# Kernel optimization log

Hardware: AMD Instinct MI355X
Metric: run time of the kernel (lower is better)

Reference implementation:

```python
import jax, jax.numpy as jnp
import numpy as np

B, T, H, V, ADIM, AMAX = 16, 1024, 512, 32000, 512, 10


def setup_inputs() -> dict:
    key = jax.random.key(0)
    ks = jax.random.split(key, 24)
    def n(k, shape, s=0.05):
        return jax.random.normal(k, shape, jnp.float32) * s
    return {
        "instruction": jax.random.randint(ks[0], (B, T), 0, V, dtype=jnp.int32),
        "emb": n(ks[1], (V, H)),
        "wih_f": n(ks[2], (4 * H, H)), "whh_f": n(ks[3], (4 * H, H)),
        "bih_f": n(ks[4], (4 * H,)), "bhh_f": n(ks[5], (4 * H,)),
        "wih_b": n(ks[6], (4 * H, H)), "whh_b": n(ks[7], (4 * H, H)),
        "bih_b": n(ks[8], (4 * H,)), "bhh_b": n(ks[9], (4 * H,)),
        "wg": n(ks[10], (2 * H, 2 * H)), "bg": n(ks[11], (2 * H,)),
        "ws1": n(ks[12], (H, 2 * H)), "bs1": n(ks[13], (H,)),
        "ws2": n(ks[14], (1, H)), "bs2": n(ks[15], (1,)),
        "wd1": n(ks[16], (H, 2 * H)), "bd1": n(ks[17], (H,)),
        "wd2": n(ks[18], (ADIM, H)), "bd2": n(ks[19], (ADIM,)),
        "max_actions": AMAX,
    }


def _lstm(x, wih, whh, bias):
    # x: [B, T, H] -> outputs [B, T, H]; PyTorch gate order i, f, g, o
    h0 = jnp.zeros((x.shape[0], whh.shape[1]), x.dtype)
    def step(carry, xt):
        h, c = carry
        g = xt @ wih.T + h @ whh.T + bias
        i, f, gg, o = jnp.split(g, 4, axis=-1)
        c = jax.nn.sigmoid(f) * c + jax.nn.sigmoid(i) * jnp.tanh(gg)
        h = jax.nn.sigmoid(o) * jnp.tanh(c)
        return (h, c), h
    _, hs = jax.lax.scan(step, (h0, h0), jnp.swapaxes(x, 0, 1))
    return jnp.swapaxes(hs, 0, 1)


def reference(instruction, emb, wih_f, whh_f, bih_f, bhh_f, wih_b, whh_b, bih_b, bhh_b,
              wg, bg, ws1, bs1, ws2, bs2, wd1, bd1, wd2, bd2, max_actions):
    x = emb[instruction]                                   # [B, T, H]
    fwd = _lstm(x, wih_f, whh_f, bih_f + bhh_f)            # [B, T, H]
    bwd = _lstm(x[:, ::-1], wih_b, whh_b, bih_b + bhh_b)[:, ::-1]
    enc = jnp.concatenate([fwd, bwd], axis=-1)             # [B, T, 2H]
    # sequence_lengths=None: h_n[0]=fwd last step, h_n[1]=bwd at t=0
    pooled = jnp.concatenate([fwd[:, -1], bwd[:, 0]], axis=-1)
    gctx = pooled @ wg.T + bg                               # [B, 2H]
    sh = jax.nn.relu(enc @ ws1.T + bs1)
    seg_probs = jax.nn.sigmoid((sh @ ws2.T + bs2)[..., 0])  # [B, T]
    mask = seg_probs > 0.5
    count = mask.sum(axis=-1)
    # first max_actions True positions per row (stable sort keeps time order)
    order = jnp.argsort(jnp.logical_not(mask), axis=1, stable=True)[:, :max_actions]
    gathered = jnp.take_along_axis(enc, order[..., None], axis=1)  # [B, A, 2H]
    slots = jnp.arange(max_actions)
    valid = slots[None, :] < jnp.minimum(count, max_actions)[:, None]
    empty = ((count == 0)[:, None]) & (slots[None, :] == 0)  # fallback: decode global ctx
    dec_in = jnp.where(valid[..., None], gathered, 0.0)
    dec_in = jnp.where(empty[..., None], gctx[:, None, :], dec_in)
    dh = jax.nn.relu(dec_in @ wd1.T + bd1)
    actions = (dh @ wd2.T + bd2) * (valid | empty)[..., None].astype(dec_in.dtype)
    return actions, seg_probs
```

## Files before the change

kernel.cpp:

```cpp
#include <hip/hip_runtime.h>
#include <math.h>

#define T   1024
#define NB  16
#define HD  512

#define OFF_BAR  0
#define OFF_HH   256
#define OFF_SH   (OFF_HH + 16777216)
#define OFF_SEGP (OFF_SH + 8388608)
#define OFF_GCTX (OFF_SEGP + 16384)
#define OFF_SEL  (OFF_GCTX + 16384)

typedef unsigned long long u64;

__device__ __forceinline__ float sigmoidf_(float x){ return 1.0f/(1.0f + __expf(-x)); }
__device__ __forceinline__ float tanhf_(float x){ return 1.0f - 2.0f/(1.0f + __expf(2.0f*x)); }

__global__ __launch_bounds__(512, 1)
void lstm_kernel(const int* __restrict__ instr, const float* __restrict__ emb,
                 const float* __restrict__ wih_f, const float* __restrict__ whh_f,
                 const float* __restrict__ bih_f, const float* __restrict__ bhh_f,
                 const float* __restrict__ wih_b, const float* __restrict__ whh_b,
                 const float* __restrict__ bih_b, const float* __restrict__ bhh_b,
                 float* __restrict__ ws)
{
    float* h_hist = ws + OFF_HH;
    int* flags = (int*)ws;

    const int wg     = blockIdx.x;
    const int dir    = wg & 1;
    const int bgrp   = (wg >> 1) & 3;
    const int uslice = wg >> 3;
    const int U      = uslice * 16;
    const int b0     = bgrp * 4;

    int* barf = flags + (dir*4 + bgrp)*32;

    const float* wih = dir ? wih_b : wih_f;
    const float* whh = dir ? whh_b : whh_f;
    const float* bih = dir ? bih_b : bih_f;
    const float* bhh = dir ? bhh_b : bhh_f;

    const int tid  = threadIdx.x;
    const int wid  = tid >> 6;
    const int lane = tid & 63;
    const int rg   = wid;

    float wi[64], wh[64];
#pragma unroll
    for (int ri = 0; ri < 8; ++ri){
        int rgl = rg*8 + ri;
        int gate = rgl >> 4, ul = rgl & 15;
        size_t row = (size_t)(gate*HD + U + ul) * HD + lane*8;
        float4 a0 = *(const float4*)(wih + row);
        float4 a1 = *(const float4*)(wih + row + 4);
        float4 b0v = *(const float4*)(whh + row);
        float4 b1v = *(const float4*)(whh + row + 4);
        wi[ri*8+0]=a0.x; wi[ri*8+1]=a0.y; wi[ri*8+2]=a0.z; wi[ri*8+3]=a0.w;
        wi[ri*8+4]=a1.x; wi[ri*8+5]=a1.y; wi[ri*8+6]=a1.z; wi[ri*8+7]=a1.w;
        wh[ri*8+0]=b0v.x; wh[ri*8+1]=b0v.y; wh[ri*8+2]=b0v.z; wh[ri*8+3]=b0v.w;
        wh[ri*8+4]=b1v.x; wh[ri*8+5]=b1v.y; wh[ri*8+6]=b1v.z; wh[ri*8+7]=b1v.w;
    }

    float bI, bF, bG, bO, cst = 0.0f;
    {
        int u = tid & 15;
        bI = bih[0*HD + U + u] + bhh[0*HD + U + u];
        bF = bih[1*HD + U + u] + bhh[1*HD + U + u];
        bG = bih[2*HD + U + u] + bhh[2*HD + U + u];
        bO = bih[3*HD + U + u] + bhh[3*HD + U + u];
    }

    __shared__ float gbuf[256];

    const int jown = ((lane&1)<<4)|((lane&2)<<2)|(lane&4)|((lane&8)>>2)|((lane&16)>>4);
    const int own_bi  = jown >> 3;
    const int own_rgl = rg*8 + (jown & 7);
    const int gslot   = (own_rgl >> 4)*64 + own_bi*16 + (own_rgl & 15);

    for (int s = 0; s < T; ++s){
        const int tp = dir ? (T-1-s) : s;

        float a[32];
#pragma unroll
        for (int j = 0; j < 32; ++j) a[j] = 0.0f;

#pragma unroll
        for (int bi = 0; bi < 4; ++bi){
            int b = b0 + bi;
            int idx = instr[b*T + tp];
            const float* px = emb + (size_t)idx*HD + lane*8;
            float4 x0 = *(const float4*)px;
            float4 x1 = *(const float4*)(px + 4);
            float xs[8] = {x0.x,x0.y,x0.z,x0.w,x1.x,x1.y,x1.z,x1.w};
#pragma unroll
            for (int kk = 0; kk < 8; ++kk){
                float xv = xs[kk];
#pragma unroll
                for (int ri = 0; ri < 8; ++ri)
                    a[bi*8+ri] = fmaf(xv, wi[ri*8+kk], a[bi*8+ri]);
            }
        }

        if (s > 0){
            if (wid == 0){
                for (;;){
                    int v = __hip_atomic_load(barf + (lane & 31), __ATOMIC_RELAXED, __HIP_MEMORY_SCOPE_AGENT);
                    if (__all(v >= s)) break;
                    __builtin_amdgcn_s_sleep(1);
                }
            }
            __syncthreads();

            const int tprev = dir ? (T - s) : (s - 1);
            const float* hbase = h_hist + (size_t)(dir*T + tprev)*NB*HD;
#pragma unroll
            for (int bi = 0; bi < 4; ++bi){
                int b = b0 + bi;
                const float* ph = hbase + (size_t)b*HD + lane*8;
                float4 h0 = *(const float4*)ph;
                float4 h1 = *(const float4*)(ph + 4);
                float hs[8] = {h0.x,h0.y,h0.z,h0.w,h1.x,h1.y,h1.z,h1.w};
#pragma unroll
                for (int kk = 0; kk < 8; ++kk){
                    float hv = hs[kk];
#pragma unroll
                    for (int ri = 0; ri < 8; ++ri)
                        a[bi*8+ri] = fmaf(hv, wh[ri*8+kk], a[bi*8+ri]);
                }
            }
        }

#pragma unroll
        for (int m = 0; m < 5; ++m){
            const int half = 16 >> m;
            const bool up = (lane >> m) & 1;
#pragma unroll
            for (int j = 0; j < 16; ++j){
                if (j < half){
                    float lo = a[j], hi = a[j+half];
                    float rlo = __shfl_xor(lo, 1<<m, 64);
                    float rhi = __shfl_xor(hi, 1<<m, 64);
                    a[j] = up ? (hi + rhi) : (lo + rlo);
                }
            }
        }
        a[0] += __shfl_xor(a[0], 32, 64);

        if ((lane & 32) == 0) gbuf[gslot] = a[0];
        __syncthreads();

        if (tid < 64){
            float iv = sigmoidf_(gbuf[      tid] + bI);
            float fv = sigmoidf_(gbuf[ 64 + tid] + bF);
            float gv = tanhf_  (gbuf[128 + tid] + bG);
            float ov = sigmoidf_(gbuf[192 + tid] + bO);
            cst = fv*cst + iv*gv;
            float hv = ov * tanhf_(cst);
            int b = b0 + (tid >> 4), u = tid & 15;
            __hip_atomic_store(&h_hist[((size_t)(dir*T + tp)*NB + b)*HD + U + u], hv,
                               __ATOMIC_RELAXED, __HIP_MEMORY_SCOPE_AGENT);
        }
        asm volatile("s_waitcnt vmcnt(0)" ::: "memory");
        __builtin_amdgcn_sched_barrier(0);
        if (tid == 0)
            __hip_atomic_store(barf + uslice, s + 1, __ATOMIC_RELAXED, __HIP_MEMORY_SCOPE_AGENT);
    }
}

__global__ __launch_bounds__(256, 2)
void seg_gemm(const float* __restrict__ ws_, const float* __restrict__ ws1,
              const float* __restrict__ bs1)
{
    const float* h_hist = ws_ + OFF_HH;
    float* SH = (float*)(ws_ + OFF_SH);
    __shared__ float As[64][17];
    __shared__ float Bs[64][17];
    const int m0 = blockIdx.x * 64;
    const int n0 = blockIdx.y * 64;
    const int tid = threadIdx.x;
    const int r  = tid >> 2;
    const int kq = (tid & 3) * 4;
    const int ty = tid >> 4, tx = tid & 15;
    const int bI = m0 >> 10;
    const int t0 = m0 & 1023;

    float acc[4][4];
#pragma unroll
    for (int i=0;i<4;i++)
#pragma unroll
        for (int j=0;j<4;j++) acc[i][j]=0.0f;

    for (int kb = 0; kb < 1024; kb += 16){
        int kk = kb + kq;
        const float* ap = (kk < 512)
            ? h_hist + ((size_t)(t0 + r)*NB + bI)*HD + kk
            : h_hist + ((size_t)(T + t0 + r)*NB + bI)*HD + (kk - 512);
        float4 av = *(const float4*)ap;
        As[r][kq+0]=av.x; As[r][kq+1]=av.y; As[r][kq+2]=av.z; As[r][kq+3]=av.w;
        float4 bv = *(const float4*)(ws1 + (size_t)(n0 + r)*1024 + kk);
        Bs[r][kq+0]=bv.x; Bs[r][kq+1]=bv.y; Bs[r][kq+2]=bv.z; Bs[r][kq+3]=bv.w;
        __syncthreads();
#pragma unroll
        for (int k2 = 0; k2 < 16; ++k2){
            float av_[4], bv_[4];
#pragma unroll
            for (int i=0;i<4;i++) av_[i] = As[ty*4+i][k2];
#pragma unroll
            for (int j=0;j<4;j++) bv_[j] = Bs[tx*4+j][k2];
#pragma unroll
            for (int i=0;i<4;i++)
#pragma unroll
                for (int j=0;j<4;j++) acc[i][j] = fmaf(av_[i], bv_[j], acc[i][j]);
        }
        __syncthreads();
    }
#pragma unroll
    for (int i=0;i<4;i++){
        int m = m0 + ty*4 + i;
#pragma unroll
        for (int j=0;j<4;j++){
            int n = n0 + tx*4 + j;
            SH[(size_t)m*512 + n] = fmaxf(acc[i][j] + bs1[n], 0.0f);
        }
    }
}

__global__ void seg_score(const float* __restrict__ ws_, const float* __restrict__ ws2,
                          const float* __restrict__ bs2, float* __restrict__ dout)
{
    const float* SH = ws_ + OFF_SH;
    float* segp = (float*)(ws_ + OFF_SEGP);
    int row  = blockIdx.x*4 + (threadIdx.x >> 6);
    int lane = threadIdx.x & 63;
    const float* p = SH + (size_t)row*512 + lane*8;
    const float* q = ws2 + lane*8;
    float4 a0=*(const float4*)p, a1=*(const float4*)(p+4);
    float4 b0=*(const float4*)q, b1=*(const float4*)(q+4);
    float ssum = a0.x*b0.x + a0.y*b0.y + a0.z*b0.z + a0.w*b0.w
               + a1.x*b1.x + a1.y*b1.y + a1.z*b1.z + a1.w*b1.w;
#pragma unroll
    for (int m=1;m<64;m<<=1) ssum += __shfl_xor(ssum, m, 64);
    if (lane == 0){
        float z = ssum + bs2[0];
        float pr = 1.0f/(1.0f + __expf(-z));
        segp[row] = pr;
        dout[81920 + row] = pr;
    }
}

__global__ void select_gctx(float* __restrict__ ws_, const float* __restrict__ wgm,
                            const float* __restrict__ bgv)
{
    const float* h_hist = ws_ + OFF_HH;
    const float* segp   = ws_ + OFF_SEGP;
    float* gctx = ws_ + OFF_GCTX;
    int* sel = (int*)(ws_ + OFF_SEL);
    int b = blockIdx.x, tid = threadIdx.x;
    __shared__ unsigned char flag[1024];
    __shared__ float pool[1024];
    for (int j = tid; j < 1024; j += 256){
        flag[j] = segp[b*1024 + j] > 0.5f ? 1 : 0;
        pool[j] = (j < 512) ? h_hist[((size_t)1023*NB + b)*HD + j]
                            : h_hist[((size_t)T*NB + b)*HD + (j - 512)];
    }
    __syncthreads();
    if (tid == 0){
        int c = 0;
        int tmp[10];
        for (int j = 0; j < 10; ++j) tmp[j] = 0;
        for (int t = 0; t < 1024; ++t){
            if (flag[t]){ if (c < 10) tmp[c] = t; c++; }
        }
        for (int j = 0; j < 10; ++j) sel[b*12 + j] = tmp[j];
        sel[b*12 + 10] = c;
        sel[b*12 + 11] = 0;
    }
    __syncthreads();
    for (int n = tid; n < 1024; n += 256){
        float acc = bgv[n];
        const float* wr = wgm + (size_t)n*1024;
        for (int k = 0; k < 1024; k += 4){
            acc += wr[k]*pool[k] + wr[k+1]*pool[k+1] + wr[k+2]*pool[k+2] + wr[k+3]*pool[k+3];
        }
        gctx[b*1024 + n] = acc;
    }
}

__global__ void decode(const float* __restrict__ ws_, const float* __restrict__ wd1,
                       const float* __restrict__ bd1, const float* __restrict__ wd2,
                       const float* __restrict__ bd2, float* __restrict__ dout)
{
    const float* h_hist = ws_ + OFF_HH;
    const float* gctx   = ws_ + OFF_GCTX;
    const int* sel = (const int*)(ws_ + OFF_SEL);
    int blk = blockIdx.x;
    int b = blk / 10, slot = blk % 10;
    int tid = threadIdx.x;
    int count = sel[b*12 + 10];
    int nval = count < 10 ? count : 10;
    bool empty = (count == 0);
    float* outp = dout + (size_t)(b*10 + slot)*512;
    if (slot >= nval && !(empty && slot == 0)){
        for (int n = tid; n < 512; n += 256) outp[n] = 0.0f;
        return;
    }
    __shared__ float row[1024];
    __shared__ float dh[512];
    if (empty){
        for (int j = tid; j < 1024; j += 256) row[j] = gctx[b*1024 + j];
    } else {
        int t = sel[b*12 + slot];
        for (int j = tid; j < 1024; j += 256)
            row[j] = (j < 512) ? h_hist[((size_t)t*NB + b)*HD + j]
                               : h_hist[((size_t)(T + t)*NB + b)*HD + (j-512)];
    }
    __syncthreads();
    for (int d = tid; d < 512; d += 256){
        float acc = bd1[d];
        const float* wr = wd1 + (size_t)d*1024;
        for (int k = 0; k < 1024; ++k) acc += wr[k]*row[k];
        dh[d] = fmaxf(acc, 0.0f);
    }
    __syncthreads();
    for (int n = tid; n < 512; n += 256){
        float acc = bd2[n];
        const float* wr = wd2 + (size_t)n*512;
        for (int k = 0; k < 512; ++k) acc += wr[k]*dh[k];
        outp[n] = acc;
    }
}

extern "C" void kernel_launch(void* const* d_in, const int* in_sizes, int n_in,
                              void* d_out, int out_size, void* d_ws, size_t ws_size,
                              hipStream_t stream)
{
    const int*   instr = (const int*)d_in[0];
    const float* emb   = (const float*)d_in[1];
    const float* wih_f = (const float*)d_in[2];
    const float* whh_f = (const float*)d_in[3];
    const float* bih_f = (const float*)d_in[4];
    const float* bhh_f = (const float*)d_in[5];
    const float* wih_b = (const float*)d_in[6];
    const float* whh_b = (const float*)d_in[7];
    const float* bih_b = (const float*)d_in[8];
    const float* bhh_b = (const float*)d_in[9];
    const float* wg_   = (const float*)d_in[10];
    const float* bg_   = (const float*)d_in[11];
    const float* ws1   = (const float*)d_in[12];
    const float* bs1   = (const float*)d_in[13];
    const float* ws2   = (const float*)d_in[14];
    const float* bs2   = (const float*)d_in[15];
    const float* wd1   = (const float*)d_in[16];
    const float* bd1   = (const float*)d_in[17];
    const float* wd2   = (const float*)d_in[18];
    const float* bd2   = (const float*)d_in[19];
    float* out = (float*)d_out;
    float* ws  = (float*)d_ws;

    hipMemsetAsync(d_ws, 0, 1024, stream);

    hipLaunchKernelGGL(lstm_kernel, dim3(256), dim3(512), 0, stream,
                       instr, emb, wih_f, whh_f, bih_f, bhh_f,
                       wih_b, whh_b, bih_b, bhh_b, ws);
    hipLaunchKernelGGL(seg_gemm, dim3(256, 8), dim3(256), 0, stream, ws, ws1, bs1);
    hipLaunchKernelGGL(seg_score, dim3(4096), dim3(256), 0, stream, ws, ws2, bs2, out);
    hipLaunchKernelGGL(select_gctx, dim3(16), dim3(256), 0, stream, ws, wg_, bg_);
    hipLaunchKernelGGL(decode, dim3(160), dim3(256), 0, stream, ws, wd1, bd1, wd2, bd2, out);
}
```

Baseline: 4.465 ms.

## Replace flag barrier with sentinel-polled hidden-state data in LSTM recurrence

The per-step cross-workgroup flag barrier is removed. The h history buffer is pre-filled with a 0xFFFFFFFF sentinel, and one wave polls the previous step's hidden values directly until none are sentinel, then stages them in shared memory for the whole block. This cuts the flag store, the vmcnt wait and a separate load round trip from each step's critical path. In exchange, a 64 MB memset runs before every call, and it relies on an h value never being exactly the NaN sentinel bit pattern.

```diff
diff --git a/kernel.cpp b/kernel.cpp
--- a/kernel.cpp
+++ b/kernel.cpp
@@ -26,7 +26,6 @@
                  float* __restrict__ ws)
 {
     float* h_hist = ws + OFF_HH;
-    int* flags = (int*)ws;
 
     const int wg     = blockIdx.x;
     const int dir    = wg & 1;
@@ -34,8 +33,6 @@
     const int uslice = wg >> 3;
     const int U      = uslice * 16;
     const int b0     = bgrp * 4;
-
-    int* barf = flags + (dir*4 + bgrp)*32;
 
     const float* wih = dir ? wih_b : wih_f;
     const float* whh = dir ? whh_b : whh_f;
@@ -72,6 +69,7 @@
         bO = bih[3*HD + U + u] + bhh[3*HD + U + u];
     }
 
+    __shared__ float hxch[8*4*64];
     __shared__ float gbuf[256];
 
     const int jown = ((lane&1)<<4)|((lane&2)<<2)|(lane&4)|((lane&8)>>2)|((lane&16)>>4);
@@ -104,24 +102,45 @@
         }
 
         if (s > 0){
+            const int tprev = dir ? (T - s) : (s - 1);
+            const float* hbase = h_hist + (size_t)(dir*T + tprev)*NB*HD;
+
             if (wid == 0){
+                u64 pq[16];
                 for (;;){
-                    int v = __hip_atomic_load(barf + (lane & 31), __ATOMIC_RELAXED, __HIP_MEMORY_SCOPE_AGENT);
-                    if (__all(v >= s)) break;
+#pragma unroll
+                    for (int bi = 0; bi < 4; ++bi){
+                        const u64* p = (const u64*)(hbase + (size_t)(b0+bi)*HD + lane*8);
+#pragma unroll
+                        for (int q = 0; q < 4; ++q)
+                            pq[bi*4+q] = __hip_atomic_load(p + q, __ATOMIC_RELAXED, __HIP_MEMORY_SCOPE_AGENT);
+                    }
+                    unsigned ok = 1u;
+#pragma unroll
+                    for (int j = 0; j < 16; ++j){
+                        ok &= ((unsigned)(pq[j]      ) != 0xFFFFFFFFu) ? 1u : 0u;
+                        ok &= ((unsigned)(pq[j] >> 32) != 0xFFFFFFFFu) ? 1u : 0u;
+                    }
+                    if (__all(ok != 0u)) break;
                     __builtin_amdgcn_s_sleep(1);
+                }
+#pragma unroll
+                for (int bi = 0; bi < 4; ++bi){
+#pragma unroll
+                    for (int q = 0; q < 4; ++q){
+                        hxch[(2*q  )*256 + bi*64 + lane] = __uint_as_float((unsigned)(pq[bi*4+q]      ));
+                        hxch[(2*q+1)*256 + bi*64 + lane] = __uint_as_float((unsigned)(pq[bi*4+q] >> 32));
+                    }
                 }
             }
             __syncthreads();
 
-            const int tprev = dir ? (T - s) : (s - 1);
-            const float* hbase = h_hist + (size_t)(dir*T + tprev)*NB*HD;
 #pragma unroll
             for (int bi = 0; bi < 4; ++bi){
-                int b = b0 + bi;
-                const float* ph = hbase + (size_t)b*HD + lane*8;
-                float4 h0 = *(const float4*)ph;
-                float4 h1 = *(const float4*)(ph + 4);
-                float hs[8] = {h0.x,h0.y,h0.z,h0.w,h1.x,h1.y,h1.z,h1.w};
+                float hs[8];
+#pragma unroll
+                for (int kk = 0; kk < 8; ++kk)
+                    hs[kk] = hxch[kk*256 + bi*64 + lane];
 #pragma unroll
                 for (int kk = 0; kk < 8; ++kk){
                     float hv = hs[kk];
@@ -162,10 +181,6 @@
             __hip_atomic_store(&h_hist[((size_t)(dir*T + tp)*NB + b)*HD + U + u], hv,
                                __ATOMIC_RELAXED, __HIP_MEMORY_SCOPE_AGENT);
         }
-        asm volatile("s_waitcnt vmcnt(0)" ::: "memory");
-        __builtin_amdgcn_sched_barrier(0);
-        if (tid == 0)
-            __hip_atomic_store(barf + uslice, s + 1, __ATOMIC_RELAXED, __HIP_MEMORY_SCOPE_AGENT);
     }
 }
 
@@ -359,7 +374,7 @@
     float* out = (float*)d_out;
     float* ws  = (float*)d_ws;
 
-    hipMemsetAsync(d_ws, 0, 1024, stream);
+    hipMemsetAsync((char*)d_ws + (size_t)OFF_HH*4, 0xFF, (size_t)16777216*4, stream);
 
     hipLaunchKernelGGL(lstm_kernel, dim3(256), dim3(512), 0, stream,
                        instr, emb, wih_f, whh_f, bih_f, bhh_f,
```

Measured after the change: 4.390 ms. Within noise of the previous version (-1.7%).

## Interleave forward and backward LSTM directions in each workgroup to hide barrier latency

Applied to the files above, without the earlier changes.

Each workgroup now owns 8 hidden units for both directions instead of 16 units for one direction. Each step alternates forward and backward half-steps, so one direction's grid-barrier wait overlaps the other direction's compute and gate math. Embedding rows for the next step are prefetched into registers. Each half-step does half the FMA work per direction, and the change adds more syncthreads, 64-slot barrier flags and a larger workspace offset and memset.

```diff
diff --git a/kernel.cpp b/kernel.cpp
--- a/kernel.cpp
+++ b/kernel.cpp
@@ -6,7 +6,7 @@
 #define HD  512
 
 #define OFF_BAR  0
-#define OFF_HH   256
+#define OFF_HH   768
 #define OFF_SH   (OFF_HH + 16777216)
 #define OFF_SEGP (OFF_SH + 8388608)
 #define OFF_GCTX (OFF_SEGP + 16384)
@@ -29,96 +29,116 @@
     int* flags = (int*)ws;
 
     const int wg     = blockIdx.x;
-    const int dir    = wg & 1;
-    const int bgrp   = (wg >> 1) & 3;
-    const int uslice = wg >> 3;
-    const int U      = uslice * 16;
+    const int bgrp   = wg & 3;
+    const int uslice = wg >> 2;
+    const int U      = uslice * 8;
     const int b0     = bgrp * 4;
 
-    int* barf = flags + (dir*4 + bgrp)*32;
-
-    const float* wih = dir ? wih_b : wih_f;
-    const float* whh = dir ? whh_b : whh_f;
-    const float* bih = dir ? bih_b : bih_f;
-    const float* bhh = dir ? bhh_b : bhh_f;
+    int* barfA = flags + (0*4 + bgrp)*64;
+    int* barfB = flags + (1*4 + bgrp)*64;
 
     const int tid  = threadIdx.x;
     const int wid  = tid >> 6;
     const int lane = tid & 63;
-    const int rg   = wid;
-
-    float wi[64], wh[64];
-#pragma unroll
-    for (int ri = 0; ri < 8; ++ri){
-        int rgl = rg*8 + ri;
-        int gate = rgl >> 4, ul = rgl & 15;
+
+    float wiA[32], whA[32], wiB[32], whB[32];
+#pragma unroll
+    for (int ri = 0; ri < 4; ++ri){
+        int r = wid*4 + ri;
+        int gate = r >> 3, ul = r & 7;
         size_t row = (size_t)(gate*HD + U + ul) * HD + lane*8;
-        float4 a0 = *(const float4*)(wih + row);
-        float4 a1 = *(const float4*)(wih + row + 4);
-        float4 b0v = *(const float4*)(whh + row);
-        float4 b1v = *(const float4*)(whh + row + 4);
-        wi[ri*8+0]=a0.x; wi[ri*8+1]=a0.y; wi[ri*8+2]=a0.z; wi[ri*8+3]=a0.w;
-        wi[ri*8+4]=a1.x; wi[ri*8+5]=a1.y; wi[ri*8+6]=a1.z; wi[ri*8+7]=a1.w;
-        wh[ri*8+0]=b0v.x; wh[ri*8+1]=b0v.y; wh[ri*8+2]=b0v.z; wh[ri*8+3]=b0v.w;
-        wh[ri*8+4]=b1v.x; wh[ri*8+5]=b1v.y; wh[ri*8+6]=b1v.z; wh[ri*8+7]=b1v.w;
-    }
-
-    float bI, bF, bG, bO, cst = 0.0f;
-    {
-        int u = tid & 15;
-        bI = bih[0*HD + U + u] + bhh[0*HD + U + u];
-        bF = bih[1*HD + U + u] + bhh[1*HD + U + u];
-        bG = bih[2*HD + U + u] + bhh[2*HD + U + u];
-        bO = bih[3*HD + U + u] + bhh[3*HD + U + u];
-    }
-
-    __shared__ float gbuf[256];
-
-    const int jown = ((lane&1)<<4)|((lane&2)<<2)|(lane&4)|((lane&8)>>2)|((lane&16)>>4);
-    const int own_bi  = jown >> 3;
-    const int own_rgl = rg*8 + (jown & 7);
-    const int gslot   = (own_rgl >> 4)*64 + own_bi*16 + (own_rgl & 15);
+        float4 a0 = *(const float4*)(wih_f + row);
+        float4 a1 = *(const float4*)(wih_f + row + 4);
+        wiA[ri*8+0]=a0.x; wiA[ri*8+1]=a0.y; wiA[ri*8+2]=a0.z; wiA[ri*8+3]=a0.w;
+        wiA[ri*8+4]=a1.x; wiA[ri*8+5]=a1.y; wiA[ri*8+6]=a1.z; wiA[ri*8+7]=a1.w;
+        float4 b0v = *(const float4*)(whh_f + row);
+        float4 b1v = *(const float4*)(whh_f + row + 4);
+        whA[ri*8+0]=b0v.x; whA[ri*8+1]=b0v.y; whA[ri*8+2]=b0v.z; whA[ri*8+3]=b0v.w;
+        whA[ri*8+4]=b1v.x; whA[ri*8+5]=b1v.y; whA[ri*8+6]=b1v.z; whA[ri*8+7]=b1v.w;
+        float4 c0 = *(const float4*)(wih_b + row);
+        float4 c1 = *(const float4*)(wih_b + row + 4);
+        wiB[ri*8+0]=c0.x; wiB[ri*8+1]=c0.y; wiB[ri*8+2]=c0.z; wiB[ri*8+3]=c0.w;
+        wiB[ri*8+4]=c1.x; wiB[ri*8+5]=c1.y; wiB[ri*8+6]=c1.z; wiB[ri*8+7]=c1.w;
+        float4 d0 = *(const float4*)(whh_b + row);
+        float4 d1 = *(const float4*)(whh_b + row + 4);
+        whB[ri*8+0]=d0.x; whB[ri*8+1]=d0.y; whB[ri*8+2]=d0.z; whB[ri*8+3]=d0.w;
+        whB[ri*8+4]=d1.x; whB[ri*8+5]=d1.y; whB[ri*8+6]=d1.z; whB[ri*8+7]=d1.w;
+    }
+
+    const float* bihX = (wid == 7) ? bih_b : bih_f;
+    const float* bhhX = (wid == 7) ? bhh_b : bhh_f;
+    const int ug = U + (lane & 7);
+    const float bI = bihX[0*HD + ug] + bhhX[0*HD + ug];
+    const float bF = bihX[1*HD + ug] + bhhX[1*HD + ug];
+    const float bG = bihX[2*HD + ug] + bhhX[2*HD + ug];
+    const float bO = bihX[3*HD + ug] + bhhX[3*HD + ug];
+    float cst = 0.0f;
+
+    __shared__ float gbuf[128];
+
+    const int jown = ((lane&1)<<3)|((lane&2)<<1)|((lane&4)>>1)|((lane&8)>>3);
+    const int own_bi  = jown >> 2;
+    const int own_row = wid*4 + (jown & 3);
+    const int gslot   = (own_row >> 3)*32 + own_bi*8 + (own_row & 7);
+
+    float4 xA[8], xB[8];
+#pragma unroll
+    for (int bi = 0; bi < 4; ++bi){
+        int idx = instr[(b0+bi)*T + 0];
+        const float* px = emb + (size_t)idx*HD + lane*8;
+        xA[bi*2]   = *(const float4*)px;
+        xA[bi*2+1] = *(const float4*)(px + 4);
+    }
 
     for (int s = 0; s < T; ++s){
-        const int tp = dir ? (T-1-s) : s;
-
-        float a[32];
-#pragma unroll
-        for (int j = 0; j < 32; ++j) a[j] = 0.0f;
-
+        const int tpA = s;
+        const int tpB = T-1-s;
+        float a[16];
+
+#pragma unroll
+        for (int j = 0; j < 16; ++j) a[j] = 0.0f;
 #pragma unroll
         for (int bi = 0; bi < 4; ++bi){
-            int b = b0 + bi;
-            int idx = instr[b*T + tp];
-            const float* px = emb + (size_t)idx*HD + lane*8;
-            float4 x0 = *(const float4*)px;
-            float4 x1 = *(const float4*)(px + 4);
-            float xs[8] = {x0.x,x0.y,x0.z,x0.w,x1.x,x1.y,x1.z,x1.w};
+            float xs[8] = {xA[bi*2].x,xA[bi*2].y,xA[bi*2].z,xA[bi*2].w,
+                           xA[bi*2+1].x,xA[bi*2+1].y,xA[bi*2+1].z,xA[bi*2+1].w};
 #pragma unroll
             for (int kk = 0; kk < 8; ++kk){
                 float xv = xs[kk];
 #pragma unroll
-                for (int ri = 0; ri < 8; ++ri)
-                    a[bi*8+ri] = fmaf(xv, wi[ri*8+kk], a[bi*8+ri]);
-            }
-        }
+                for (int ri = 0; ri < 4; ++ri)
+                    a[bi*4+ri] = fmaf(xv, wiA[ri*8+kk], a[bi*4+ri]);
+            }
+        }
+
+        if (s > 0 && wid == 7){
+            asm volatile("s_waitcnt vmcnt(0)" ::: "memory");
+            __builtin_amdgcn_sched_barrier(0);
+            if (lane == 0)
+                __hip_atomic_store(barfB + uslice, s, __ATOMIC_RELAXED, __HIP_MEMORY_SCOPE_AGENT);
+        }
+
+#pragma unroll
+        for (int bi = 0; bi < 4; ++bi){
+            int idx = instr[(b0+bi)*T + tpB];
+            const float* px = emb + (size_t)idx*HD + lane*8;
+            xB[bi*2]   = *(const float4*)px;
+            xB[bi*2+1] = *(const float4*)(px + 4);
+        }
+
+        if (s > 0 && wid == 0){
+            for (;;){
+                int v = __hip_atomic_load(barfA + lane, __ATOMIC_RELAXED, __HIP_MEMORY_SCOPE_AGENT);
+                if (__all(v >= s)) break;
+                __builtin_amdgcn_s_sleep(1);
+            }
+        }
+        __syncthreads();
 
         if (s > 0){
-            if (wid == 0){
-                for (;;){
-                    int v = __hip_atomic_load(barf + (lane & 31), __ATOMIC_RELAXED, __HIP_MEMORY_SCOPE_AGENT);
-                    if (__all(v >= s)) break;
-                    __builtin_amdgcn_s_sleep(1);
-                }
-            }
-            __syncthreads();
-
-            const int tprev = dir ? (T - s) : (s - 1);
-            const float* hbase = h_hist + (size_t)(dir*T + tprev)*NB*HD;
+            const float* hbase = h_hist + (size_t)(s-1)*NB*HD;
 #pragma unroll
             for (int bi = 0; bi < 4; ++bi){
-                int b = b0 + bi;
-                const float* ph = hbase + (size_t)b*HD + lane*8;
+                const float* ph = hbase + (size_t)(b0+bi)*HD + lane*8;
                 float4 h0 = *(const float4*)ph;
                 float4 h1 = *(const float4*)(ph + 4);
                 float hs[8] = {h0.x,h0.y,h0.z,h0.w,h1.x,h1.y,h1.z,h1.w};
@@ -126,18 +146,18 @@
                 for (int kk = 0; kk < 8; ++kk){
                     float hv = hs[kk];
 #pragma unroll
-                    for (int ri = 0; ri < 8; ++ri)
-                        a[bi*8+ri] = fmaf(hv, wh[ri*8+kk], a[bi*8+ri]);
+                    for (int ri = 0; ri < 4; ++ri)
+                        a[bi*4+ri] = fmaf(hv, whA[ri*8+kk], a[bi*4+ri]);
                 }
             }
         }
 
 #pragma unroll
-        for (int m = 0; m < 5; ++m){
-            const int half = 16 >> m;
+        for (int m = 0; m < 4; ++m){
+            const int half = 8 >> m;
             const bool up = (lane >> m) & 1;
 #pragma unroll
-            for (int j = 0; j < 16; ++j){
+            for (int j = 0; j < 8; ++j){
                 if (j < half){
                     float lo = a[j], hi = a[j+half];
                     float rlo = __shfl_xor(lo, 1<<m, 64);
@@ -146,26 +166,116 @@
                 }
             }
         }
+        a[0] += __shfl_xor(a[0], 16, 64);
         a[0] += __shfl_xor(a[0], 32, 64);
-
-        if ((lane & 32) == 0) gbuf[gslot] = a[0];
-        __syncthreads();
-
-        if (tid < 64){
-            float iv = sigmoidf_(gbuf[      tid] + bI);
-            float fv = sigmoidf_(gbuf[ 64 + tid] + bF);
-            float gv = tanhf_  (gbuf[128 + tid] + bG);
-            float ov = sigmoidf_(gbuf[192 + tid] + bO);
-            cst = fv*cst + iv*gv;
-            float hv = ov * tanhf_(cst);
-            int b = b0 + (tid >> 4), u = tid & 15;
-            __hip_atomic_store(&h_hist[((size_t)(dir*T + tp)*NB + b)*HD + U + u], hv,
-                               __ATOMIC_RELAXED, __HIP_MEMORY_SCOPE_AGENT);
-        }
-        asm volatile("s_waitcnt vmcnt(0)" ::: "memory");
-        __builtin_amdgcn_sched_barrier(0);
-        if (tid == 0)
-            __hip_atomic_store(barf + uslice, s + 1, __ATOMIC_RELAXED, __HIP_MEMORY_SCOPE_AGENT);
+        if (lane < 16) gbuf[gslot] = a[0];
+        __syncthreads();
+
+        if (wid == 6){
+            if (lane < 32){
+                float iv = sigmoidf_(gbuf[      lane] + bI);
+                float fv = sigmoidf_(gbuf[ 32 + lane] + bF);
+                float gv = tanhf_  (gbuf[ 64 + lane] + bG);
+                float ov = sigmoidf_(gbuf[ 96 + lane] + bO);
+                cst = fv*cst + iv*gv;
+                float hv = ov * tanhf_(cst);
+                int b = b0 + (lane >> 3), ul = lane & 7;
+                __hip_atomic_store(&h_hist[((size_t)tpA*NB + b)*HD + U + ul], hv,
+                                   __ATOMIC_RELAXED, __HIP_MEMORY_SCOPE_AGENT);
+            }
+        }
+
+#pragma unroll
+        for (int j = 0; j < 16; ++j) a[j] = 0.0f;
+#pragma unroll
+        for (int bi = 0; bi < 4; ++bi){
+            float xs[8] = {xB[bi*2].x,xB[bi*2].y,xB[bi*2].z,xB[bi*2].w,
+                           xB[bi*2+1].x,xB[bi*2+1].y,xB[bi*2+1].z,xB[bi*2+1].w};
+#pragma unroll
+            for (int kk = 0; kk < 8; ++kk){
+                float xv = xs[kk];
+#pragma unroll
+                for (int ri = 0; ri < 4; ++ri)
+                    a[bi*4+ri] = fmaf(xv, wiB[ri*8+kk], a[bi*4+ri]);
+            }
+        }
+
+        if (wid == 6){
+            asm volatile("s_waitcnt vmcnt(0)" ::: "memory");
+            __builtin_amdgcn_sched_barrier(0);
+            if (lane == 0)
+                __hip_atomic_store(barfA + uslice, s + 1, __ATOMIC_RELAXED, __HIP_MEMORY_SCOPE_AGENT);
+        }
+
+        if (s > 0 && wid == 0){
+            for (;;){
+                int v = __hip_atomic_load(barfB + lane, __ATOMIC_RELAXED, __HIP_MEMORY_SCOPE_AGENT);
+                if (__all(v >= s)) break;
+                __builtin_amdgcn_s_sleep(1);
+            }
+        }
+        __syncthreads();
+
+        if (s + 1 < T){
+#pragma unroll
+            for (int bi = 0; bi < 4; ++bi){
+                int idx = instr[(b0+bi)*T + (s+1)];
+                const float* px = emb + (size_t)idx*HD + lane*8;
+                xA[bi*2]   = *(const float4*)px;
+                xA[bi*2+1] = *(const float4*)(px + 4);
+            }
+        }
+
+        if (s > 0){
+            const float* hbase = h_hist + (size_t)(T + (T - s))*NB*HD;
+#pragma unroll
+            for (int bi = 0; bi < 4; ++bi){
+                const float* ph = hbase + (size_t)(b0+bi)*HD + lane*8;
+                float4 h0 = *(const float4*)ph;
+                float4 h1 = *(const float4*)(ph + 4);
+                float hs[8] = {h0.x,h0.y,h0.z,h0.w,h1.x,h1.y,h1.z,h1.w};
+#pragma unroll
+                for (int kk = 0; kk < 8; ++kk){
+                    float hv = hs[kk];
+#pragma unroll
+                    for (int ri = 0; ri < 4; ++ri)
+                        a[bi*4+ri] = fmaf(hv, whB[ri*8+kk], a[bi*4+ri]);
+                }
+            }
+        }
+
+#pragma unroll
+        for (int m = 0; m < 4; ++m){
+            const int half = 8 >> m;
+            const bool up = (lane >> m) & 1;
+#pragma unroll
+            for (int j = 0; j < 8; ++j){
+                if (j < half){
+                    float lo = a[j], hi = a[j+half];
+                    float rlo = __shfl_xor(lo, 1<<m, 64);
+                    float rhi = __shfl_xor(hi, 1<<m, 64);
+                    a[j] = up ? (hi + rhi) : (lo + rlo);
+                }
+            }
+        }
+        a[0] += __shfl_xor(a[0], 16, 64);
+        a[0] += __shfl_xor(a[0], 32, 64);
+        if (lane < 16) gbuf[gslot] = a[0];
+        __syncthreads();
+
+        if (wid == 7){
+            if (lane < 32){
+                float iv = sigmoidf_(gbuf[      lane] + bI);
+                float fv = sigmoidf_(gbuf[ 32 + lane] + bF);
+                float gv = tanhf_  (gbuf[ 64 + lane] + bG);
+                float ov = sigmoidf_(gbuf[ 96 + lane] + bO);
+                cst = fv*cst + iv*gv;
+                float hv = ov * tanhf_(cst);
+                int b = b0 + (lane >> 3), ul = lane & 7;
+                __hip_atomic_store(&h_hist[((size_t)(T + tpB)*NB + b)*HD + U + ul], hv,
+                                   __ATOMIC_RELAXED, __HIP_MEMORY_SCOPE_AGENT);
+            }
+        }
     }
 }
 
@@ -359,7 +469,7 @@
     float* out = (float*)d_out;
     float* ws  = (float*)d_ws;
 
-    hipMemsetAsync(d_ws, 0, 1024, stream);
+    hipMemsetAsync(d_ws, 0, 2048, stream);
 
     hipLaunchKernelGGL(lstm_kernel, dim3(256), dim3(512), 0, stream,
                        instr, emb, wih_f, whh_f, bih_f, bhh_f,
```

New measurement: 6.364 ms. 1.43x slower.

## Remove intra-block barriers in LSTM step with per-wave flags and shuffle-based gate math

Applied to the files above, without the earlier changes.

Each wave now owns two hidden units with all four of their gates, so the gate nonlinearities are computed in-wave after a shuffle exchange. This removes the shared-memory gbuf and both __syncthreads per timestep. The cross-block barrier now uses one flag per wave instead of one per block, and every wave polls all 256 flags itself with 64-bit loads. The goal is to cut intra-block synchronisation latency on the serial recurrent critical path. The cost is heavier flag polling traffic from every wave and a larger flag region.

```diff
diff --git a/kernel.cpp b/kernel.cpp
--- a/kernel.cpp
+++ b/kernel.cpp
@@ -6,7 +6,7 @@
 #define HD  512
 
 #define OFF_BAR  0
-#define OFF_HH   256
+#define OFF_HH   2048
 #define OFF_SH   (OFF_HH + 16777216)
 #define OFF_SEGP (OFF_SH + 8388608)
 #define OFF_GCTX (OFF_SEGP + 16384)
@@ -35,7 +35,7 @@
     const int U      = uslice * 16;
     const int b0     = bgrp * 4;
 
-    int* barf = flags + (dir*4 + bgrp)*32;
+    int* barf = flags + (dir*4 + bgrp)*256;
 
     const float* wih = dir ? wih_b : wih_f;
     const float* whh = dir ? whh_b : whh_f;
@@ -45,14 +45,12 @@
     const int tid  = threadIdx.x;
     const int wid  = tid >> 6;
     const int lane = tid & 63;
-    const int rg   = wid;
 
     float wi[64], wh[64];
 #pragma unroll
     for (int ri = 0; ri < 8; ++ri){
-        int rgl = rg*8 + ri;
-        int gate = rgl >> 4, ul = rgl & 15;
-        size_t row = (size_t)(gate*HD + U + ul) * HD + lane*8;
+        int gate = ri >> 1, ui = ri & 1;
+        size_t row = (size_t)(gate*HD + U + wid*2 + ui) * HD + lane*8;
         float4 a0 = *(const float4*)(wih + row);
         float4 a1 = *(const float4*)(wih + row + 4);
         float4 b0v = *(const float4*)(whh + row);
@@ -63,21 +61,20 @@
         wh[ri*8+4]=b1v.x; wh[ri*8+5]=b1v.y; wh[ri*8+6]=b1v.z; wh[ri*8+7]=b1v.w;
     }
 
-    float bI, bF, bG, bO, cst = 0.0f;
-    {
-        int u = tid & 15;
-        bI = bih[0*HD + U + u] + bhh[0*HD + U + u];
-        bF = bih[1*HD + U + u] + bhh[1*HD + U + u];
-        bG = bih[2*HD + U + u] + bhh[2*HD + U + u];
-        bO = bih[3*HD + U + u] + bhh[3*HD + U + u];
-    }
-
-    __shared__ float gbuf[256];
-
-    const int jown = ((lane&1)<<4)|((lane&2)<<2)|(lane&4)|((lane&8)>>2)|((lane&16)>>4);
-    const int own_bi  = jown >> 3;
-    const int own_rgl = rg*8 + (jown & 7);
-    const int gslot   = (own_rgl >> 4)*64 + own_bi*16 + (own_rgl & 15);
+    const int j0 = ((lane&1)<<4)|((lane&2)<<2)|(lane&4)|((lane&8)>>2)|((lane&16)>>4);
+    const bool own = ((lane & 12) == 0) && (lane < 32);
+    const int own_bi = j0 >> 3;
+    const int own_ui = j0 & 1;
+    const int own_u  = U + wid*2 + own_ui;
+    const int own_b  = b0 + own_bi;
+
+    const float bI = bih[0*HD + own_u] + bhh[0*HD + own_u];
+    const float bF = bih[1*HD + own_u] + bhh[1*HD + own_u];
+    const float bG = bih[2*HD + own_u] + bhh[2*HD + own_u];
+    const float bO = bih[3*HD + own_u] + bhh[3*HD + own_u];
+    float cst = 0.0f;
+
+    const u64* fb = (const u64*)barf;
 
     for (int s = 0; s < T; ++s){
         const int tp = dir ? (T-1-s) : s;
@@ -104,21 +101,20 @@
         }
 
         if (s > 0){
-            if (wid == 0){
-                for (;;){
-                    int v = __hip_atomic_load(barf + (lane & 31), __ATOMIC_RELAXED, __HIP_MEMORY_SCOPE_AGENT);
-                    if (__all(v >= s)) break;
-                    __builtin_amdgcn_s_sleep(1);
-                }
+            for (;;){
+                u64 q0 = __hip_atomic_load(fb + lane*2,     __ATOMIC_RELAXED, __HIP_MEMORY_SCOPE_AGENT);
+                u64 q1 = __hip_atomic_load(fb + lane*2 + 1, __ATOMIC_RELAXED, __HIP_MEMORY_SCOPE_AGENT);
+                bool ok = ((int)(q0      ) >= s) && ((int)(q0 >> 32) >= s)
+                       && ((int)(q1      ) >= s) && ((int)(q1 >> 32) >= s);
+                if (__all(ok)) break;
+                __builtin_amdgcn_s_sleep(1);
             }
-            __syncthreads();
 
             const int tprev = dir ? (T - s) : (s - 1);
             const float* hbase = h_hist + (size_t)(dir*T + tprev)*NB*HD;
 #pragma unroll
             for (int bi = 0; bi < 4; ++bi){
-                int b = b0 + bi;
-                const float* ph = hbase + (size_t)b*HD + lane*8;
+                const float* ph = hbase + (size_t)(b0+bi)*HD + lane*8;
                 float4 h0 = *(const float4*)ph;
                 float4 h1 = *(const float4*)(ph + 4);
                 float hs[8] = {h0.x,h0.y,h0.z,h0.w,h1.x,h1.y,h1.z,h1.w};
@@ -148,24 +144,31 @@
         }
         a[0] += __shfl_xor(a[0], 32, 64);
 
-        if ((lane & 32) == 0) gbuf[gslot] = a[0];
-        __syncthreads();
-
-        if (tid < 64){
-            float iv = sigmoidf_(gbuf[      tid] + bI);
-            float fv = sigmoidf_(gbuf[ 64 + tid] + bF);
-            float gv = tanhf_  (gbuf[128 + tid] + bG);
-            float ov = sigmoidf_(gbuf[192 + tid] + bO);
-            cst = fv*cst + iv*gv;
-            float hv = ov * tanhf_(cst);
-            int b = b0 + (tid >> 4), u = tid & 15;
-            __hip_atomic_store(&h_hist[((size_t)(dir*T + tp)*NB + b)*HD + U + u], hv,
-                               __ATOMIC_RELAXED, __HIP_MEMORY_SCOPE_AGENT);
-        }
+        float vi = a[0];
+        float vf = __shfl_xor(vi, 8, 64);
+        float vg = __shfl_xor(vi, 4, 64);
+        float vo = __shfl_xor(vi, 12, 64);
+
+        float iv = sigmoidf_(vi + bI);
+        float fv = sigmoidf_(vf + bF);
+        float gv = tanhf_  (vg + bG);
+        float ov = sigmoidf_(vo + bO);
+        cst = fv*cst + iv*gv;
+        float hv = ov * tanhf_(cst);
+
+        float hv2 = __shfl_xor(hv, 16, 64);
+        if (own && own_ui == 0){
+            float2 pr = make_float2(hv, hv2);
+            __hip_atomic_store(
+                (u64*)&h_hist[((size_t)(dir*T + tp)*NB + own_b)*HD + U + wid*2],
+                __builtin_bit_cast(u64, pr), __ATOMIC_RELAXED, __HIP_MEMORY_SCOPE_AGENT);
+        }
+
         asm volatile("s_waitcnt vmcnt(0)" ::: "memory");
         __builtin_amdgcn_sched_barrier(0);
-        if (tid == 0)
-            __hip_atomic_store(barf + uslice, s + 1, __ATOMIC_RELAXED, __HIP_MEMORY_SCOPE_AGENT);
+        if (lane == 0)
+            __hip_atomic_store(barf + uslice*8 + wid, s + 1,
+                               __ATOMIC_RELAXED, __HIP_MEMORY_SCOPE_AGENT);
     }
 }
 
@@ -359,7 +362,7 @@
     float* out = (float*)d_out;
     float* ws  = (float*)d_ws;
 
-    hipMemsetAsync(d_ws, 0, 1024, stream);
+    hipMemsetAsync(d_ws, 0, 8192, stream);
 
     hipLaunchKernelGGL(lstm_kernel, dim3(256), dim3(512), 0, stream,
                        instr, emb, wih_f, whh_f, bih_f, bhh_f,
```

After: 8.878 ms. 98.8% more time.
